# Kernel optimization log

Measured on AMD Instinct MI355X. Metric: run time of the kernel, lower is better.

## Reference

```python
import jax, jax.numpy as jnp
from jax import lax
import numpy as np

B, IMG = 64, 224
NUM_CLASSES, FEAT, HID, OUT = 80, 1024, 512, 256
TOP_K, KNN = 2, 4
N_NODES = 5  # full, object, component, detail, remaining (each a single row per sample)


def setup_inputs() -> dict:
    ks = jax.random.split(jax.random.key(0), 8)
    s = 0.02
    f32 = jnp.float32
    return {
        "x": jax.random.normal(ks[0], (B, 3, IMG, IMG), f32),
        "conv1_w": jax.random.normal(ks[1], (32, 3, 3, 3), f32) * s,
        "conv1_b": jnp.zeros((32,), f32),
        "conv2_w": jax.random.normal(ks[2], (64, 32, 3, 3), f32) * s,
        "conv2_b": jnp.zeros((64,), f32),
        "fcf_w": jax.random.normal(ks[3], (64, FEAT), f32) * s,
        "fcf_b": jnp.zeros((FEAT,), f32),
        "fcc_w": jax.random.normal(ks[4], (FEAT, NUM_CLASSES), f32) * s,
        "fcc_b": jnp.zeros((NUM_CLASSES,), f32),
        "gnn_w1": jax.random.normal(ks[5], (NUM_CLASSES, FEAT, HID), f32) * s,
        "gnn_b1": jnp.zeros((NUM_CLASSES, HID), f32),
        "gnn_w2": jax.random.normal(ks[6], (NUM_CLASSES, HID, OUT), f32) * s,
        "gnn_b2": jnp.zeros((NUM_CLASSES, OUT), f32),
        "fin_w": jax.random.normal(ks[7], (OUT, NUM_CLASSES), f32) * s,
        "fin_b": jnp.zeros((NUM_CLASSES,), f32),
    }


def _gcn_norm(A_hat):
    # A_hat[..., t, s] already contains self loops; symmetric normalization D^-1/2 A D^-1/2
    deg = A_hat.sum(-1)
    dinv = jnp.where(deg > 0, lax.rsqrt(deg), 0.0)
    return A_hat * dinv[..., :, None] * dinv[..., None, :]


def reference(x, conv1_w, conv1_b, conv2_w, conv2_b, fcf_w, fcf_b, fcc_w, fcc_b,
              gnn_w1, gnn_b1, gnn_w2, gnn_b2, fin_w, fin_b):
    dn = ("NCHW", "OIHW", "NCHW")
    # --- YOLO backbone: 2 strided convs + GAP + FC heads ---
    h = jax.nn.relu(lax.conv_general_dilated(x, conv1_w, (2, 2), "SAME", dimension_numbers=dn)
                    + conv1_b[None, :, None, None])
    h = jax.nn.relu(lax.conv_general_dilated(h, conv2_w, (2, 2), "SAME", dimension_numbers=dn)
                    + conv2_b[None, :, None, None])
    pooled = h.mean((2, 3))                                  # [B, 64]
    feats = jax.nn.relu(pooled @ fcf_w + fcf_b)              # [B, FEAT]
    logits = feats @ fcc_w + fcc_b                           # [B, NUM_CLASSES]
    top_idx = lax.top_k(logits, TOP_K)[1]                    # [B, K]

    # --- hierarchical 5-node graph per sample (vectorized over batch) ---
    s4 = FEAT // 4
    pad_to = lambda v: jnp.pad(v, ((0, 0), (0, FEAT - v.shape[1])))
    Xg = jnp.stack([feats,
                    pad_to(feats[:, :s4]),
                    pad_to(feats[:, s4:2 * s4]),
                    pad_to(feats[:, 2 * s4:3 * s4]),
                    pad_to(feats[:, 3 * s4:])], axis=1)      # [B, 5, FEAT]

    d2 = jnp.sum((Xg[:, :, None, :] - Xg[:, None, :, :]) ** 2, -1)   # [B, 5, 5]
    nbr = lax.top_k(-d2, KNN)[1]                                      # knn_graph, loop=True
    A = jax.nn.one_hot(nbr, N_NODES, dtype=Xg.dtype).sum(2)          # [B, 5, 5], A[t, s]
    An = _gcn_norm(A + jnp.eye(N_NODES, dtype=Xg.dtype))             # GCNConv adds self loops

    # --- top-k expert GNNs: gather expert weights, 2-layer GCN + global mean pool ---
    w1, b1 = gnn_w1[top_idx], gnn_b1[top_idx]                        # [B,K,FEAT,HID], [B,K,HID]
    w2, b2 = gnn_w2[top_idx], gnn_b2[top_idx]
    agg = jnp.einsum("bts,bsf->btf", An, Xg)                          # propagate once, shared
    h1 = jax.nn.relu(jnp.einsum("btf,bkfh->bkth", agg, w1) + b1[:, :, None, :])
    h2 = jnp.einsum("bts,bksh->bkth", An, h1)
    h2 = jnp.einsum("bkth,bkho->bkto", h2, w2) + b2[:, :, None, :]
    g = h2.mean(2)                                                    # global mean pool [B,K,OUT]

    # --- final GCNConv over stacked expert outputs, reusing LAST sample's edge_index ---
    comb = g.reshape(B * TOP_K, OUT)
    Af = jnp.eye(B * TOP_K, dtype=comb.dtype)                         # self loops on all N nodes
    Af = Af.at[:N_NODES, :N_NODES].add(A[-1])                         # last sample's knn edges
    fin = _gcn_norm(Af) @ (comb @ fin_w) + fin_b                      # [B*K, NUM_CLASSES]
    return fin.reshape(B, TOP_K, NUM_CLASSES).mean(1)
```

## Files before the change

kernel.cpp:

```cpp
#include <hip/hip_runtime.h>


typedef float f32x4 __attribute__((ext_vector_type(4)));

__global__ void k_prep(const float* __restrict__ w1, const float* __restrict__ w2,
                       float* __restrict__ wt1, float* __restrict__ wt2,
                       float* __restrict__ pooled) {
    int i = blockIdx.x * 256 + threadIdx.x;
    if (i < 4096) pooled[i] = 0.f;
    if (i < 864) {
        int k = i >> 5, co = i & 31;
        wt1[i] = w1[co * 27 + k];
    }
    if (i < 18432) {
        int co = i & 63, tt = i >> 6;
        int kx = tt % 3, u = tt / 3;
        int ci = u & 31, ky = u >> 5;
        wt2[i] = w2[co * 288 + ci * 9 + ky * 3 + kx];
    }
}

__global__ __launch_bounds__(256) void k_conv1(const float* __restrict__ x,
                                               const float* __restrict__ wt1,
                                               const float* __restrict__ bias,
                                               float* __restrict__ out) {
    int gid = blockIdx.x * 256 + threadIdx.x;
    int ox = gid % 112;
    int t = gid / 112;
    int oy = t % 112;
    int b = t / 112;
    float acc[32];
#pragma unroll
    for (int i = 0; i < 32; i++) acc[i] = 0.f;
    const float* xb = x + (size_t)b * 3 * 224 * 224;
#pragma unroll
    for (int ky = 0; ky < 3; ky++) {
        int iy = 2 * oy + ky;
#pragma unroll
        for (int kx = 0; kx < 3; kx++) {
            int ix = 2 * ox + kx;
            bool ok = (iy < 224) && (ix < 224);
#pragma unroll
            for (int ci = 0; ci < 3; ci++) {
                float v = ok ? xb[((size_t)ci * 224 + iy) * 224 + ix] : 0.f;
                const float* w = wt1 + ((ci * 3 + ky) * 3 + kx) * 32;
#pragma unroll
                for (int co = 0; co < 32; co++) acc[co] = fmaf(v, w[co], acc[co]);
            }
        }
    }
    float* ob = out + (size_t)b * 32 * 12544 + oy * 112 + ox;
#pragma unroll
    for (int co = 0; co < 32; co++) {
        float r = acc[co] + bias[co];
        ob[(size_t)co * 12544] = r > 0.f ? r : 0.f;
    }
}

__global__ __launch_bounds__(256) void k_conv2gap(const float* __restrict__ h1,
                                                  const float* __restrict__ wt2,
                                                  const float* __restrict__ b2,
                                                  float* __restrict__ pooled) {
    __shared__ float s[16][5][116];
    int oy2 = blockIdx.x;
    int b = blockIdx.y;
    int tid = threadIdx.x;

    int q = __builtin_amdgcn_readfirstlane((int)(tid >> 6));
    int lane = tid & 63;
    bool pvld = lane < 56;
    int opx = pvld ? lane : 55;
    float acc[2][16];
#pragma unroll
    for (int ry = 0; ry < 2; ry++)
#pragma unroll
        for (int j = 0; j < 16; j++) acc[ry][j] = 0.f;

#pragma unroll 1
    for (int cp = 0; cp < 2; cp++) {
        if (cp) __syncthreads();
        for (int i = tid; i < 2320; i += 256) {
            int row = i / 29, f4 = i - row * 29;
            int ci = row / 5, r = row - ci * 5;
            int iy = 4 * oy2 + r;
            float4 v = make_float4(0.f, 0.f, 0.f, 0.f);
            if (f4 < 28 && iy < 112)
                v = *(const float4*)&h1[(((size_t)b * 32 + cp * 16 + ci) * 112 + iy) * 112 + 4 * f4];
            *(float4*)&s[ci][r][4 * f4] = v;
        }
        __syncthreads();

#pragma unroll
        for (int ky = 0; ky < 3; ky++) {
#pragma unroll 4
            for (int ci = 0; ci < 16; ci++) {
                const float* w = wt2 + ((ky * 32 + cp * 16 + ci) * 3) * 64 + q * 16;
#pragma unroll
                for (int ry = 0; ry < 2; ry++) {
                    int r = 2 * ry + ky;
                    float2 v01 = *(const float2*)&s[ci][r][2 * opx];
                    float v2 = s[ci][r][2 * opx + 2];
#pragma unroll
                    for (int j = 0; j < 16; j++) acc[ry][j] = fmaf(v01.x, w[j], acc[ry][j]);
#pragma unroll
                    for (int j = 0; j < 16; j++) acc[ry][j] = fmaf(v01.y, w[64 + j], acc[ry][j]);
#pragma unroll
                    for (int j = 0; j < 16; j++) acc[ry][j] = fmaf(v2, w[128 + j], acc[ry][j]);
                }
            }
        }
    }
#pragma unroll
    for (int j = 0; j < 16; j++) {
        float bj = b2[q * 16 + j];
        float rv = 0.f;
        if (pvld)
            rv = fmaxf(acc[0][j] + bj, 0.f) + fmaxf(acc[1][j] + bj, 0.f);
#pragma unroll
        for (int sft = 32; sft > 0; sft >>= 1) rv += __shfl_xor(rv, sft);
        if (lane == 0) atomicAdd(&pooled[b * 64 + q * 16 + j], rv);
    }
}

__global__ __launch_bounds__(256) void k_mid(const float* __restrict__ pooled,
                                             const float* __restrict__ fcf_w,
                                             const float* __restrict__ fcf_b,
                                             const float* __restrict__ fcc_w,
                                             const float* __restrict__ fcc_b,
                                             int* __restrict__ top_idx,
                                             float* __restrict__ cm,
                                             int* __restrict__ dropped,
                                             float* __restrict__ agg) {
    __shared__ float sf[1024];
    __shared__ float slog[2][80];
    __shared__ float sr[10][4];
    __shared__ float sAn[25];
    int b = blockIdx.x, t = threadIdx.x;

    {
        float acc[4];
#pragma unroll
        for (int j = 0; j < 4; j++) acc[j] = fcf_b[t + j * 256];
        for (int cc = 0; cc < 64; cc++) {
            float pv = pooled[b * 64 + cc] * (1.f / 3136.f);
#pragma unroll
            for (int j = 0; j < 4; j++)
                acc[j] = fmaf(pv, fcf_w[cc * 1024 + t + j * 256], acc[j]);
        }
#pragma unroll
        for (int j = 0; j < 4; j++) sf[t + j * 256] = fmaxf(acc[j], 0.f);
    }
    __syncthreads();

    if (t < 160) {
        int c = t % 80, half = t / 80;
        float acc = half ? 0.f : fcc_b[c];
        for (int f = half * 512; f < half * 512 + 512; f++)
            acc = fmaf(sf[f], fcc_w[f * 80 + c], acc);
        slog[half][c] = acc;
    }
    {
        float q1 = sf[t], q2 = sf[256 + t], q3 = sf[512 + t], q4 = sf[768 + t];
        float part[10] = {q1 * q1, q2 * q2, q3 * q3, q4 * q4,
                          q1 * q2, q1 * q3, q1 * q4, q2 * q3, q2 * q4, q3 * q4};
        int lane = t & 63, wid = t >> 6;
#pragma unroll
        for (int i = 0; i < 10; i++) {
            float r = part[i];
#pragma unroll
            for (int sft = 32; sft > 0; sft >>= 1) r += __shfl_xor(r, sft);
            if (lane == 0) sr[i][wid] = r;
        }
    }
    __syncthreads();

    if (t < 64) {
        int ln = t;
        float vA = slog[0][ln] + slog[1][ln];
        int iA = ln;
        bool hasB = ln < 16;
        float vB = hasB ? slog[0][64 + ln] + slog[1][64 + ln] : -3.4e38f;
        int iB = hasB ? 64 + ln : 0x7fffffff;
        float v1, v2; int i1, i2;
        if (vB > vA) { v1 = vB; i1 = iB; v2 = vA; i2 = iA; }
        else         { v1 = vA; i1 = iA; v2 = vB; i2 = iB; }
#pragma unroll
        for (int m = 1; m < 64; m <<= 1) {
            float o1 = __shfl_xor(v1, m), o2 = __shfl_xor(v2, m);
            int oi1 = __shfl_xor(i1, m), oi2 = __shfl_xor(i2, m);
            bool selfWins = (v1 > o1) || (v1 == o1 && i1 < oi1);
            float n1, n2; int ni1, ni2;
            if (selfWins) {
                n1 = v1; ni1 = i1;
                bool s2 = (v2 > o1) || (v2 == o1 && i2 < oi1);
                n2 = s2 ? v2 : o1; ni2 = s2 ? i2 : oi1;
            } else {
                n1 = o1; ni1 = oi1;
                bool s2 = (v1 > o2) || (v1 == o2 && i1 < oi2);
                n2 = s2 ? v1 : o2; ni2 = s2 ? i1 : oi2;
            }
            v1 = n1; i1 = ni1; v2 = n2; i2 = ni2;
        }
        if (ln == 0) { top_idx[b * 2] = i1; top_idx[b * 2 + 1] = i2; }
    }
    if (t == 0) {
        float tot[10];
#pragma unroll
        for (int i = 0; i < 10; i++) tot[i] = sr[i][0] + sr[i][1] + sr[i][2] + sr[i][3];
        float n_[5] = {0.f, tot[0], tot[1], tot[2], tot[3]};
        float dd[5][5];
        dd[1][1] = tot[0]; dd[2][2] = tot[1]; dd[3][3] = tot[2]; dd[4][4] = tot[3];
        dd[1][2] = dd[2][1] = tot[4]; dd[1][3] = dd[3][1] = tot[5];
        dd[1][4] = dd[4][1] = tot[6]; dd[2][3] = dd[3][2] = tot[7];
        dd[2][4] = dd[4][2] = tot[8]; dd[3][4] = dd[4][3] = tot[9];
        float Q = tot[0] + tot[1] + tot[2] + tot[3];
        float d2[5][5];
        d2[0][0] = 0.f;
        for (int i = 1; i < 5; i++) {
            float v = Q + n_[i] - 2.f * dd[1][i];
            d2[0][i] = v; d2[i][0] = v;
        }
        for (int i = 1; i < 5; i++)
            for (int j = 1; j < 5; j++)
                d2[i][j] = (i == j) ? 0.f : (n_[i] + n_[j] - 2.f * dd[i][j]);
        int drp[5];
        for (int r = 0; r < 5; r++) {
            int dm = 0; float vm = d2[r][0];
            for (int ss = 1; ss < 5; ss++)
                if (d2[r][ss] >= vm) { vm = d2[r][ss]; dm = ss; }
            drp[r] = dm;
            dropped[b * 5 + r] = dm;
        }
        float dinv[5], Ah[5][5];
        for (int r = 0; r < 5; r++) {
            float dsum = 0.f;
            for (int ss = 0; ss < 5; ss++) {
                float a = ((ss != drp[r]) ? 1.f : 0.f) + ((ss == r) ? 1.f : 0.f);
                Ah[r][ss] = a; dsum += a;
            }
            dinv[r] = dsum > 0.f ? 1.f / sqrtf(dsum) : 0.f;
        }
        float colsum[5] = {0.f, 0.f, 0.f, 0.f, 0.f};
        for (int r = 0; r < 5; r++)
            for (int ss = 0; ss < 5; ss++) {
                float v = Ah[r][ss] * dinv[r] * dinv[ss];
                sAn[r * 5 + ss] = v;
                colsum[ss] += v;
            }
        for (int ss = 0; ss < 5; ss++) cm[b * 5 + ss] = colsum[ss] * 0.2f;
    }
    __syncthreads();

    for (int f = t; f < 1024; f += 256) {
        float a0 = sf[f];
        bool inq = f < 256;
        float v1 = 0.f, v2 = 0.f, v3 = 0.f, v4 = 0.f;
        if (inq) { v1 = sf[f]; v2 = sf[256 + f]; v3 = sf[512 + f]; v4 = sf[768 + f]; }
#pragma unroll
        for (int tt = 0; tt < 5; tt++) {
            float r = sAn[tt * 5] * a0;
            if (inq)
                r += sAn[tt * 5 + 1] * v1 + sAn[tt * 5 + 2] * v2 +
                     sAn[tt * 5 + 3] * v3 + sAn[tt * 5 + 4] * v4;
            agg[((size_t)b * 5 + tt) * 1024 + f] = r;
        }
    }
}

__global__ __launch_bounds__(128) void k_h1part(const float* __restrict__ agg,
                                                const float* __restrict__ w1,
                                                const int* __restrict__ top_idx,
                                                float* __restrict__ h1part) {
    int pair = blockIdx.x;
    int fc = blockIdx.y;
    int hg = threadIdx.x;
    int bsm = pair >> 1;
    int c = top_idx[pair];
    const f32x4* wv = (const f32x4*)(w1 + (size_t)c * 1024 * 512);
    const f32x4* av = (const f32x4*)(agg + (size_t)bsm * 5 * 1024);
    f32x4 acc[5];
#pragma unroll
    for (int t = 0; t < 5; t++) acc[t] = (f32x4)(0.f);
    int f0 = fc * 128;
#pragma unroll 2
    for (int f4 = 0; f4 < 32; f4++) {
        f32x4 a[5];
#pragma unroll
        for (int t = 0; t < 5; t++) a[t] = av[t * 256 + fc * 32 + f4];
#pragma unroll
        for (int j = 0; j < 4; j++) {
            f32x4 w = wv[(size_t)(f0 + f4 * 4 + j) * 128 + hg];
#pragma unroll
            for (int t = 0; t < 5; t++) acc[t] += a[t][j] * w;
        }
    }
    float* op = h1part + (((size_t)fc * 128 + pair) * 5) * 512;
#pragma unroll
    for (int t = 0; t < 5; t++)
        *(f32x4*)(op + t * 512 + 4 * hg) = acc[t];
}

__global__ __launch_bounds__(512) void k_expert2(const float* __restrict__ h1part,
                                                 const float* __restrict__ b1,
                                                 const float* __restrict__ w2,
                                                 const float* __restrict__ b2,
                                                 const float* __restrict__ finw,
                                                 const float* __restrict__ cm,
                                                 const int* __restrict__ top_idx,
                                                 float* __restrict__ M) {
    __shared__ float sp[512];
    __shared__ float sgq[8][256];
    __shared__ float sgg[256];
    int pair = blockIdx.x, t = threadIdx.x;
    int bsm = pair >> 1;
    int c = top_idx[pair];

    {
        float pv = 0.f;
#pragma unroll
        for (int tt = 0; tt < 5; tt++) {
            float sv = 0.f;
#pragma unroll
            for (int fc = 0; fc < 8; fc++)
                sv += h1part[(((size_t)fc * 128 + pair) * 5 + tt) * 512 + t];
            float hv = fmaxf(sv + b1[c * 512 + t], 0.f);
            pv = fmaf(cm[bsm * 5 + tt], hv, pv);
        }
        sp[t] = pv;
    }
    __syncthreads();

    {
        int og = t & 63, hq = t >> 6;
        const f32x4* wv2 = (const f32x4*)(w2 + (size_t)c * 512 * 256);
        f32x4 acc2 = (f32x4)(0.f);
#pragma unroll 4
        for (int h = hq * 64; h < hq * 64 + 64; h++)
            acc2 += sp[h] * wv2[(size_t)h * 64 + og];
        *(f32x4*)&sgq[hq][og * 4] = acc2;
    }
    __syncthreads();
    if (t < 64) {
        f32x4 gsum = *(const f32x4*)&sgq[0][t * 4];
#pragma unroll
        for (int hq = 1; hq < 8; hq++) gsum += *(const f32x4*)&sgq[hq][t * 4];
        gsum += *(const f32x4*)&b2[c * 256 + 4 * t];
        *(f32x4*)&sgg[4 * t] = gsum;
    }
    __syncthreads();
    if (t < 80) {
        float acc3 = 0.f;
        for (int o = 0; o < 256; o++) acc3 = fmaf(sgg[o], finw[o * 80 + t], acc3);
        M[pair * 80 + t] = acc3;
    }
}

__global__ __launch_bounds__(128) void k_out(const float* __restrict__ M,
                                             const float* __restrict__ finb,
                                             const int* __restrict__ dropped,
                                             float* __restrict__ out) {
    int b = blockIdx.x;
    int c = threadIdx.x;
    if (c >= 80) return;
    float bias = finb[c];
    float r = 0.f;
#pragma unroll
    for (int k = 0; k < 2; k++) {
        int n = b * 2 + k;
        float fin;
        if (n < 5) {
            float s = 0.f;
            for (int m = 0; m < 5; m++) {
                float a = ((m != dropped[63 * 5 + n]) ? 1.f : 0.f) + ((m == n) ? 1.f : 0.f);
                s += a * M[m * 80 + c];
            }
            fin = s * 0.2f + bias;
        } else {
            fin = M[n * 80 + c] + bias;
        }
        r += fin;
    }
    out[b * 80 + c] = r * 0.5f;
}

extern "C" void kernel_launch(void* const* d_in, const int* in_sizes, int n_in,
                              void* d_out, int out_size, void* d_ws, size_t ws_size,
                              hipStream_t stream) {
    const float* x       = (const float*)d_in[0];
    const float* conv1_w = (const float*)d_in[1];
    const float* conv1_b = (const float*)d_in[2];
    const float* conv2_w = (const float*)d_in[3];
    const float* conv2_b = (const float*)d_in[4];
    const float* fcf_w   = (const float*)d_in[5];
    const float* fcf_b   = (const float*)d_in[6];
    const float* fcc_w   = (const float*)d_in[7];
    const float* fcc_b   = (const float*)d_in[8];
    const float* gnn_w1  = (const float*)d_in[9];
    const float* gnn_b1  = (const float*)d_in[10];
    const float* gnn_w2  = (const float*)d_in[11];
    const float* gnn_b2  = (const float*)d_in[12];
    const float* fin_w   = (const float*)d_in[13];
    const float* fin_b   = (const float*)d_in[14];
    float* out = (float*)d_out;

    char* ws = (char*)d_ws;
    size_t off = 0;
    auto alloc = [&](size_t bytes) {
        void* pp = ws + off;
        off = (off + bytes + 255) & ~(size_t)255;
        return pp;
    };
    float* h1conv  = (float*)alloc((size_t)64 * 32 * 112 * 112 * 4);
    float* wt1     = (float*)alloc(864 * 4);
    float* wt2     = (float*)alloc(18432 * 4);
    float* pooled  = (float*)alloc(4096 * 4);
    int*   top_idx = (int*)alloc(128 * 4);
    float* cm      = (float*)alloc(320 * 4);
    int*   dropped = (int*)alloc(320 * 4);
    float* agg     = (float*)alloc(327680 * 4);
    float* h1part  = (float*)alloc((size_t)2621440 * 4);
    float* Mm      = (float*)alloc(10240 * 4);
    (void)ws_size; (void)in_sizes; (void)n_in; (void)out_size;

    k_prep<<<72, 256, 0, stream>>>(conv1_w, conv2_w, wt1, wt2, pooled);
    k_conv1<<<3136, 256, 0, stream>>>(x, wt1, conv1_b, h1conv);
    k_conv2gap<<<dim3(28, 64), 256, 0, stream>>>(h1conv, wt2, conv2_b, pooled);
    k_mid<<<64, 256, 0, stream>>>(pooled, fcf_w, fcf_b, fcc_w, fcc_b,
                                  top_idx, cm, dropped, agg);
    k_h1part<<<dim3(128, 8), 128, 0, stream>>>(agg, gnn_w1, top_idx, h1part);
    k_expert2<<<128, 512, 0, stream>>>(h1part, gnn_b1, gnn_w2, gnn_b2,
                                       fin_w, cm, top_idx, Mm);
    k_out<<<64, 128, 0, stream>>>(Mm, fin_b, dropped, out);
}
```

Before: 503.9 us.

## Tile conv1 input through LDS and split expert second layer across blocks

conv1 now stages a strip of 9 input rows per channel in shared memory with float4 loads, and each block computes 4 output rows, so overlapping stride-2 windows reuse LDS instead of re-reading global memory. The expert second-layer kernel is split into a per-hidden-chunk partial kernel (128x8 blocks) plus a fold kernel, which spreads the w2 streaming over more workgroups at the cost of an extra launch and a partial-sum buffer. The fc classifier loops also read shared features as vec4. In conv1 only 224 of 256 threads do compute, and each runs two output pixels.

After: 466.6 us. 1.08x faster.

```diff
diff --git a/kernel.cpp b/kernel.cpp
--- a/kernel.cpp
+++ b/kernel.cpp
@@ -24,36 +24,53 @@
                                                const float* __restrict__ wt1,
                                                const float* __restrict__ bias,
                                                float* __restrict__ out) {
-    int gid = blockIdx.x * 256 + threadIdx.x;
-    int ox = gid % 112;
-    int t = gid / 112;
-    int oy = t % 112;
-    int b = t / 112;
-    float acc[32];
-#pragma unroll
-    for (int i = 0; i < 32; i++) acc[i] = 0.f;
+    __shared__ float s[3][9][228];
+    int oy4 = blockIdx.x;
+    int b = blockIdx.y;
+    int tid = threadIdx.x;
     const float* xb = x + (size_t)b * 3 * 224 * 224;
-#pragma unroll
-    for (int ky = 0; ky < 3; ky++) {
-        int iy = 2 * oy + ky;
-#pragma unroll
-        for (int kx = 0; kx < 3; kx++) {
-            int ix = 2 * ox + kx;
-            bool ok = (iy < 224) && (ix < 224);
-#pragma unroll
-            for (int ci = 0; ci < 3; ci++) {
-                float v = ok ? xb[((size_t)ci * 224 + iy) * 224 + ix] : 0.f;
-                const float* w = wt1 + ((ci * 3 + ky) * 3 + kx) * 32;
-#pragma unroll
-                for (int co = 0; co < 32; co++) acc[co] = fmaf(v, w[co], acc[co]);
-            }
-        }
-    }
-    float* ob = out + (size_t)b * 32 * 12544 + oy * 112 + ox;
-#pragma unroll
-    for (int co = 0; co < 32; co++) {
-        float r = acc[co] + bias[co];
-        ob[(size_t)co * 12544] = r > 0.f ? r : 0.f;
+
+    for (int i = tid; i < 1539; i += 256) {
+        int ci = i / 513, rem = i - ci * 513;
+        int r = rem / 57, f4 = rem - r * 57;
+        int iy = 8 * oy4 + r;
+        float4 v = make_float4(0.f, 0.f, 0.f, 0.f);
+        if (iy < 224 && f4 < 56)
+            v = *(const float4*)&xb[((size_t)ci * 224 + iy) * 224 + 4 * f4];
+        *(float4*)&s[ci][r][4 * f4] = v;
+    }
+    __syncthreads();
+
+#pragma unroll 1
+    for (int rep = 0; rep < 2; rep++) {
+        int j = tid + rep * 224;
+        if (tid < 224 && j < 448) {
+            int ry = j / 112, ox = j - ry * 112;
+            float acc[32];
+#pragma unroll
+            for (int co = 0; co < 32; co++) acc[co] = 0.f;
+#pragma unroll
+            for (int ky = 0; ky < 3; ky++) {
+                int r = 2 * ry + ky;
+#pragma unroll
+                for (int kx = 0; kx < 3; kx++) {
+#pragma unroll
+                    for (int ci = 0; ci < 3; ci++) {
+                        float v = s[ci][r][2 * ox + kx];
+                        const float* w = wt1 + ((ci * 3 + ky) * 3 + kx) * 32;
+#pragma unroll
+                        for (int co = 0; co < 32; co++) acc[co] = fmaf(v, w[co], acc[co]);
+                    }
+                }
+            }
+            int oy = 4 * oy4 + ry;
+            float* ob = out + (size_t)b * 32 * 12544 + oy * 112 + ox;
+#pragma unroll
+            for (int co = 0; co < 32; co++) {
+                float rr = acc[co] + bias[co];
+                ob[(size_t)co * 12544] = rr > 0.f ? rr : 0.f;
+            }
+        }
     }
 }
 
@@ -131,7 +148,7 @@
                                              float* __restrict__ cm,
                                              int* __restrict__ dropped,
                                              float* __restrict__ agg) {
-    __shared__ float sf[1024];
+    __shared__ __align__(16) float sf[1024];
     __shared__ float slog[2][80];
     __shared__ float sr[10][4];
     __shared__ float sAn[25];
@@ -155,8 +172,13 @@
     if (t < 160) {
         int c = t % 80, half = t / 80;
         float acc = half ? 0.f : fcc_b[c];
-        for (int f = half * 512; f < half * 512 + 512; f++)
-            acc = fmaf(sf[f], fcc_w[f * 80 + c], acc);
+        int fb = half * 512;
+        for (int f4 = 0; f4 < 128; f4++) {
+            f32x4 fr = *(const f32x4*)&sf[fb + f4 * 4];
+#pragma unroll
+            for (int j = 0; j < 4; j++)
+                acc = fmaf(fr[j], fcc_w[(fb + f4 * 4 + j) * 80 + c], acc);
+        }
         slog[half][c] = acc;
     }
     {
@@ -300,20 +322,18 @@
         *(f32x4*)(op + t * 512 + 4 * hg) = acc[t];
 }
 
-__global__ __launch_bounds__(512) void k_expert2(const float* __restrict__ h1part,
-                                                 const float* __restrict__ b1,
-                                                 const float* __restrict__ w2,
-                                                 const float* __restrict__ b2,
-                                                 const float* __restrict__ finw,
-                                                 const float* __restrict__ cm,
-                                                 const int* __restrict__ top_idx,
-                                                 float* __restrict__ M) {
-    __shared__ float sp[512];
-    __shared__ float sgq[8][256];
-    __shared__ float sgg[256];
-    int pair = blockIdx.x, t = threadIdx.x;
+__global__ __launch_bounds__(64) void k_gpart(const float* __restrict__ h1part,
+                                              const float* __restrict__ b1,
+                                              const float* __restrict__ w2,
+                                              const float* __restrict__ cm,
+                                              const int* __restrict__ top_idx,
+                                              float* __restrict__ gpart) {
+    __shared__ float sp[64];
+    int pair = blockIdx.x, hc = blockIdx.y;
+    int t = threadIdx.x;
     int bsm = pair >> 1;
     int c = top_idx[pair];
+    int h = hc * 64 + t;
 
     {
         float pv = 0.f;
@@ -322,8 +342,8 @@
             float sv = 0.f;
 #pragma unroll
             for (int fc = 0; fc < 8; fc++)
-                sv += h1part[(((size_t)fc * 128 + pair) * 5 + tt) * 512 + t];
-            float hv = fmaxf(sv + b1[c * 512 + t], 0.f);
+                sv += h1part[(((size_t)fc * 128 + pair) * 5 + tt) * 512 + h];
+            float hv = fmaxf(sv + b1[c * 512 + h], 0.f);
             pv = fmaf(cm[bsm * 5 + tt], hv, pv);
         }
         sp[t] = pv;
@@ -331,27 +351,42 @@
     __syncthreads();
 
     {
-        int og = t & 63, hq = t >> 6;
         const f32x4* wv2 = (const f32x4*)(w2 + (size_t)c * 512 * 256);
-        f32x4 acc2 = (f32x4)(0.f);
+        f32x4 acc = (f32x4)(0.f);
 #pragma unroll 4
-        for (int h = hq * 64; h < hq * 64 + 64; h++)
-            acc2 += sp[h] * wv2[(size_t)h * 64 + og];
-        *(f32x4*)&sgq[hq][og * 4] = acc2;
-    }
-    __syncthreads();
-    if (t < 64) {
-        f32x4 gsum = *(const f32x4*)&sgq[0][t * 4];
-#pragma unroll
-        for (int hq = 1; hq < 8; hq++) gsum += *(const f32x4*)&sgq[hq][t * 4];
-        gsum += *(const f32x4*)&b2[c * 256 + 4 * t];
-        *(f32x4*)&sgg[4 * t] = gsum;
+        for (int hh = 0; hh < 64; hh++)
+            acc += sp[hh] * wv2[(size_t)(hc * 64 + hh) * 64 + t];
+        *(f32x4*)&gpart[((size_t)hc * 128 + pair) * 256 + 4 * t] = acc;
+    }
+}
+
+__global__ __launch_bounds__(128) void k_Mfold(const float* __restrict__ gpart,
+                                               const float* __restrict__ b2,
+                                               const float* __restrict__ finw,
+                                               const int* __restrict__ top_idx,
+                                               float* __restrict__ M) {
+    __shared__ __align__(16) float sgg[256];
+    int n = blockIdx.x, t = threadIdx.x;
+    int c = top_idx[n];
+#pragma unroll
+    for (int rep = 0; rep < 2; rep++) {
+        int o = t + rep * 128;
+        float gg = b2[c * 256 + o];
+#pragma unroll
+        for (int hc = 0; hc < 8; hc++)
+            gg += gpart[((size_t)hc * 128 + n) * 256 + o];
+        sgg[o] = gg;
     }
     __syncthreads();
     if (t < 80) {
-        float acc3 = 0.f;
-        for (int o = 0; o < 256; o++) acc3 = fmaf(sgg[o], finw[o * 80 + t], acc3);
-        M[pair * 80 + t] = acc3;
+        float acc = 0.f;
+        for (int o4 = 0; o4 < 64; o4++) {
+            f32x4 gr = *(const f32x4*)&sgg[o4 * 4];
+#pragma unroll
+            for (int j = 0; j < 4; j++)
+                acc = fmaf(gr[j], finw[(o4 * 4 + j) * 80 + t], acc);
+        }
+        M[n * 80 + t] = acc;
     }
 }
 
@@ -419,16 +454,17 @@
     int*   dropped = (int*)alloc(320 * 4);
     float* agg     = (float*)alloc(327680 * 4);
     float* h1part  = (float*)alloc((size_t)2621440 * 4);
+    float* gpart   = (float*)alloc(262144 * 4);
     float* Mm      = (float*)alloc(10240 * 4);
     (void)ws_size; (void)in_sizes; (void)n_in; (void)out_size;
 
     k_prep<<<72, 256, 0, stream>>>(conv1_w, conv2_w, wt1, wt2, pooled);
-    k_conv1<<<3136, 256, 0, stream>>>(x, wt1, conv1_b, h1conv);
+    k_conv1<<<dim3(28, 64), 256, 0, stream>>>(x, wt1, conv1_b, h1conv);
     k_conv2gap<<<dim3(28, 64), 256, 0, stream>>>(h1conv, wt2, conv2_b, pooled);
     k_mid<<<64, 256, 0, stream>>>(pooled, fcf_w, fcf_b, fcc_w, fcc_b,
                                   top_idx, cm, dropped, agg);
     k_h1part<<<dim3(128, 8), 128, 0, stream>>>(agg, gnn_w1, top_idx, h1part);
-    k_expert2<<<128, 512, 0, stream>>>(h1part, gnn_b1, gnn_w2, gnn_b2,
-                                       fin_w, cm, top_idx, Mm);
+    k_gpart<<<dim3(128, 8), 64, 0, stream>>>(h1part, gnn_b1, gnn_w2, cm, top_idx, gpart);
+    k_Mfold<<<128, 128, 0, stream>>>(gpart, gnn_b2, fin_w, top_idx, Mm);
     k_out<<<64, 128, 0, stream>>>(Mm, fin_b, dropped, out);
 }
```
